# Kernel tuning notes

Hardware: AMD Instinct MI355X
Metric: run time of the kernel (lower is better)

Reference implementation:

```python
import jax, jax.numpy as jnp
import numpy as np

TEMPERATURE = 0.5
EPS = 1e-8  # torch CosineSimilarity eps


def setup_inputs() -> dict:
    key = jax.random.key(0)
    # x holds 2*batch_size concatenated embeddings (two augmented views)
    x = jax.random.normal(key, (4096, 512), dtype=jnp.float32)
    return {"x": x}


def reference(x) -> jnp.ndarray:
    n2 = x.shape[0]          # 2N rows
    n = n2 // 2
    # cosine similarity: normalize rows (clamped norm as in torch), then GEMM
    norms = jnp.maximum(jnp.linalg.norm(x, axis=1, keepdims=True), EPS)
    xn = x / norms
    sim = jnp.einsum('id,jd->ij', xn, xn) / TEMPERATURE  # [2N, 2N]
    # positive logit for row i is sim[i, (i+N) mod 2N]
    idx = jnp.arange(n2)
    pos = sim[idx, (idx + n) % n2]
    # CE with label 0 over logits = [pos, negatives]; since the logit set for
    # row i is exactly {sim[i, j] : j != i}, CE_i = logsumexp_{j!=i} sim[i,j] - pos_i
    sim_masked = jnp.where(jnp.eye(n2, dtype=bool), -jnp.inf, sim)
    lse = jax.nn.logsumexp(sim_masked, axis=1)
    # criterion uses reduction='sum' then divides by bsz -> mean
    return jnp.mean(lse - pos)
```

## Files before the change

### kernel.cpp

```cpp
#include <hip/hip_runtime.h>
#include <hip/hip_bf16.h>
#include <math.h>

typedef __bf16 bf16_t;
typedef __bf16 bf16x8 __attribute__((ext_vector_type(8)));
typedef float f32x4 __attribute__((ext_vector_type(4)));

#define N2 4096
#define NHALF 2048
#define DIM 512
#define TEMP_INV 2.0f

__global__ __launch_bounds__(256) void k_prep(const float* __restrict__ x,
                                              bf16_t* __restrict__ xn,
                                              float* __restrict__ pos,
                                              float* __restrict__ diag,
                                              float* __restrict__ rowsum) {
    const int pair = blockIdx.x * 4 + (threadIdx.x >> 6);
    const int lane = threadIdx.x & 63;
    const int rowi = pair;
    const int rowp = pair + NHALF;

    const float4* xi = reinterpret_cast<const float4*>(x + (size_t)rowi * DIM);
    const float4* xp = reinterpret_cast<const float4*>(x + (size_t)rowp * DIM);
    float4 a0 = xi[lane * 2], a1 = xi[lane * 2 + 1];
    float4 b0 = xp[lane * 2], b1 = xp[lane * 2 + 1];

    float ssi = a0.x*a0.x + a0.y*a0.y + a0.z*a0.z + a0.w*a0.w
              + a1.x*a1.x + a1.y*a1.y + a1.z*a1.z + a1.w*a1.w;
    float ssp = b0.x*b0.x + b0.y*b0.y + b0.z*b0.z + b0.w*b0.w
              + b1.x*b1.x + b1.y*b1.y + b1.z*b1.z + b1.w*b1.w;
    float dot = a0.x*b0.x + a0.y*b0.y + a0.z*b0.z + a0.w*b0.w
              + a1.x*b1.x + a1.y*b1.y + a1.z*b1.z + a1.w*b1.w;
#pragma unroll
    for (int off = 32; off; off >>= 1) {
        ssi += __shfl_xor(ssi, off, 64);
        ssp += __shfl_xor(ssp, off, 64);
        dot += __shfl_xor(dot, off, 64);
    }
    const float ni = fmaxf(sqrtf(ssi), 1e-8f);
    const float np = fmaxf(sqrtf(ssp), 1e-8f);
    const float sci = 1.0f / ni, scp = 1.0f / np;

    float va[8] = {a0.x, a0.y, a0.z, a0.w, a1.x, a1.y, a1.z, a1.w};
    float vb[8] = {b0.x, b0.y, b0.z, b0.w, b1.x, b1.y, b1.z, b1.w};
    bf16x8 oi, op;
    float dii = 0.0f, dpp = 0.0f;
#pragma unroll
    for (int t = 0; t < 8; ++t) {
        oi[t] = (bf16_t)(va[t] * sci);
        op[t] = (bf16_t)(vb[t] * scp);
        float fi = (float)oi[t], fp_ = (float)op[t];
        dii += fi * fi;
        dpp += fp_ * fp_;
    }
    *reinterpret_cast<bf16x8*>(xn + (size_t)rowi * DIM + lane * 8) = oi;
    *reinterpret_cast<bf16x8*>(xn + (size_t)rowp * DIM + lane * 8) = op;
#pragma unroll
    for (int off = 32; off; off >>= 1) {
        dii += __shfl_xor(dii, off, 64);
        dpp += __shfl_xor(dpp, off, 64);
    }
    if (lane == 0) {
        const float pv = TEMP_INV * dot * sci * scp;
        pos[rowi] = pv;
        pos[rowp] = pv;
        diag[rowi] = TEMP_INV * dii;
        diag[rowp] = TEMP_INV * dpp;
    }
    if (threadIdx.x < 8) rowsum[blockIdx.x * 8 + threadIdx.x] = 0.0f;
}

__device__ __forceinline__ void load_lds16(const bf16_t* g, bf16_t* l) {
    __builtin_amdgcn_global_load_lds(
        (const __attribute__((address_space(1))) unsigned int*)g,
        (__attribute__((address_space(3))) unsigned int*)l,
        16, 0, 0);
}

__global__ __launch_bounds__(256) void k_simgemm(const bf16_t* __restrict__ xn,
                                                 float* __restrict__ rowsum) {
    __shared__ bf16_t As[3][128 * 32];
    __shared__ bf16_t Bs[3][128 * 32];
    __shared__ float  rpA[128];
    __shared__ float  rpB[128];

    const int t = blockIdx.x;
    int bn = (int)((sqrtf(8.0f * (float)t + 1.0f) - 1.0f) * 0.5f);
    while ((bn * (bn + 1)) / 2 > t) --bn;
    while (((bn + 1) * (bn + 2)) / 2 <= t) ++bn;
    const int bm = t - (bn * (bn + 1)) / 2;
    const bool diagb = (bm == bn);

    const int tid  = threadIdx.x;
    const int lane = tid & 63;
    const int wid  = tid >> 6;
    const int wr   = wid >> 1;
    const int wc   = wid & 1;
    const int q    = lane >> 4;
    const int l15  = lane & 15;

    if (tid < 128) { rpA[tid] = 0.0f; rpB[tid] = 0.0f; }

    const int slot_g = (tid & 3) ^ ((tid >> 3) & 3);
    const bf16_t* gA = xn + (size_t)(bm * 128 + (tid >> 2)) * DIM + slot_g * 8;
    const bf16_t* gB = xn + (size_t)(bn * 128 + (tid >> 2)) * DIM + slot_g * 8;

    const int rsw = (q ^ ((l15 >> 1) & 3)) * 8;
    const int arow = (wr * 64 + l15) * 32 + rsw;
    const int brow = (wc * 64 + l15) * 32 + rsw;

    f32x4 acc[4][4] = {};

    load_lds16(gA,                         &As[0][tid * 8]);
    load_lds16(gA + (size_t)64 * DIM,      &As[0][2048 + tid * 8]);
    load_lds16(gB,                         &Bs[0][tid * 8]);
    load_lds16(gB + (size_t)64 * DIM,      &Bs[0][2048 + tid * 8]);
    load_lds16(gA + 32,                    &As[1][tid * 8]);
    load_lds16(gA + (size_t)64 * DIM + 32, &As[1][2048 + tid * 8]);
    load_lds16(gB + 32,                    &Bs[1][tid * 8]);
    load_lds16(gB + (size_t)64 * DIM + 32, &Bs[1][2048 + tid * 8]);

#pragma unroll
    for (int kt = 0; kt < 16; ++kt) {
        if (kt < 15) asm volatile("s_waitcnt vmcnt(4)" ::: "memory");
        else         asm volatile("s_waitcnt vmcnt(0)" ::: "memory");
        __builtin_amdgcn_s_barrier();
        __builtin_amdgcn_sched_barrier(0);

        if (kt + 2 < 16) {
            const int nb = (kt + 2) % 3;
            const bf16_t* gA2 = gA + (kt + 2) * 32;
            const bf16_t* gB2 = gB + (kt + 2) * 32;
            load_lds16(gA2,                    &As[nb][tid * 8]);
            load_lds16(gA2 + (size_t)64 * DIM, &As[nb][2048 + tid * 8]);
            load_lds16(gB2,                    &Bs[nb][tid * 8]);
            load_lds16(gB2 + (size_t)64 * DIM, &Bs[nb][2048 + tid * 8]);
        }

        const int cb = kt % 3;
        bf16x8 af[4], bv[4];
#pragma unroll
        for (int mt = 0; mt < 4; ++mt)
            af[mt] = *reinterpret_cast<const bf16x8*>(&As[cb][arow + mt * 512]);
#pragma unroll
        for (int nt = 0; nt < 4; ++nt)
            bv[nt] = *reinterpret_cast<const bf16x8*>(&Bs[cb][brow + nt * 512]);
#pragma unroll
        for (int mt = 0; mt < 4; ++mt)
#pragma unroll
            for (int nt = 0; nt < 4; ++nt)
                acc[mt][nt] = __builtin_amdgcn_mfma_f32_16x16x32_bf16(
                    af[mt], bv[nt], acc[mt][nt], 0, 0, 0);
    }

    float colacc[4] = {0.0f, 0.0f, 0.0f, 0.0f};
#pragma unroll
    for (int mt = 0; mt < 4; ++mt) {
        float rowp[4] = {0.0f, 0.0f, 0.0f, 0.0f};
#pragma unroll
        for (int nt = 0; nt < 4; ++nt)
#pragma unroll
            for (int r = 0; r < 4; ++r) {
                float e = __expf(TEMP_INV * acc[mt][nt][r]);
                rowp[r] += e;
                colacc[nt] += e;
            }
#pragma unroll
        for (int r = 0; r < 4; ++r) {
            float p = rowp[r];
            p += __shfl_xor(p, 1, 64);
            p += __shfl_xor(p, 2, 64);
            p += __shfl_xor(p, 4, 64);
            p += __shfl_xor(p, 8, 64);
            if (l15 == 0) atomicAdd(&rpA[wr * 64 + mt * 16 + q * 4 + r], p);
        }
    }
    if (!diagb) {
#pragma unroll
        for (int nt = 0; nt < 4; ++nt) {
            float c = colacc[nt];
            c += __shfl_xor(c, 16, 64);
            c += __shfl_xor(c, 32, 64);
            if (q == 0) atomicAdd(&rpB[wc * 64 + nt * 16 + l15], c);
        }
    }
    __syncthreads();
    if (tid < 128) {
        atomicAdd(&rowsum[bm * 128 + tid], rpA[tid]);
    } else if (!diagb) {
        atomicAdd(&rowsum[bn * 128 + (tid - 128)], rpB[tid - 128]);
    }
}

__global__ __launch_bounds__(256) void k_finalize(const float* __restrict__ rowsum,
                                                  const float* __restrict__ pos,
                                                  const float* __restrict__ diag,
                                                  float* __restrict__ out) {
    __shared__ float red[256];
    const float4* rs4 = reinterpret_cast<const float4*>(rowsum);
    const float4* ps4 = reinterpret_cast<const float4*>(pos);
    const float4* dg4 = reinterpret_cast<const float4*>(diag);
    float s = 0.0f;
#pragma unroll
    for (int it = 0; it < 4; ++it) {
        const int i = it * 256 + threadIdx.x;
        float4 r = rs4[i];
        float4 p = ps4[i];
        float4 d = dg4[i];
        s += __logf(r.x - __expf(d.x)) - p.x;
        s += __logf(r.y - __expf(d.y)) - p.y;
        s += __logf(r.z - __expf(d.z)) - p.z;
        s += __logf(r.w - __expf(d.w)) - p.w;
    }
    red[threadIdx.x] = s;
    __syncthreads();
    for (int st = 128; st; st >>= 1) {
        if (threadIdx.x < st) red[threadIdx.x] += red[threadIdx.x + st];
        __syncthreads();
    }
    if (threadIdx.x == 0) out[0] = red[0] / (float)N2;
}

extern "C" void kernel_launch(void* const* d_in, const int* in_sizes, int n_in,
                              void* d_out, int out_size, void* d_ws, size_t ws_size,
                              hipStream_t stream) {
    (void)in_sizes; (void)n_in; (void)out_size; (void)ws_size;
    const float* x = (const float*)d_in[0];
    float* out = (float*)d_out;

    char* ws = (char*)d_ws;
    bf16_t* xn     = (bf16_t*)ws;
    float*  rowsum = (float*)(ws + (size_t)N2 * DIM * 2);
    float*  pos    = rowsum + N2;
    float*  diag   = pos + N2;

    k_prep<<<512, 256, 0, stream>>>(x, xn, pos, diag, rowsum);
    k_simgemm<<<528, 256, 0, stream>>>(xn, rowsum);
    k_finalize<<<1, 256, 0, stream>>>(rowsum, pos, diag, out);
}
```

Baseline: 78.77 us.

## Fuse finalize into GEMM via last-block reduction and extract diag/pos from tiles

Removes the separate finalize kernel by having the last GEMM block, found with an atomic counter, do the log-sum reduction. Diagonal terms are now masked to zero inside the GEMM tile instead of being subtracted later from precomputed values. The positive logits are read from the off-diagonal tile at offset 16 blocks instead of being computed in prep, which trims prep work and one kernel launch. The cost is extra branches in the exp epilogue, atomic adds for pos, and a serial tail in the last block.

```diff
diff --git a/kernel.cpp b/kernel.cpp
--- a/kernel.cpp
+++ b/kernel.cpp
@@ -10,12 +10,13 @@
 #define NHALF 2048
 #define DIM 512
 #define TEMP_INV 2.0f
+#define NBLK 528
 
 __global__ __launch_bounds__(256) void k_prep(const float* __restrict__ x,
                                               bf16_t* __restrict__ xn,
                                               float* __restrict__ pos,
-                                              float* __restrict__ diag,
-                                              float* __restrict__ rowsum) {
+                                              float* __restrict__ rowsum,
+                                              int* __restrict__ counter) {
     const int pair = blockIdx.x * 4 + (threadIdx.x >> 6);
     const int lane = threadIdx.x & 63;
     const int rowi = pair;
@@ -30,45 +31,28 @@
               + a1.x*a1.x + a1.y*a1.y + a1.z*a1.z + a1.w*a1.w;
     float ssp = b0.x*b0.x + b0.y*b0.y + b0.z*b0.z + b0.w*b0.w
               + b1.x*b1.x + b1.y*b1.y + b1.z*b1.z + b1.w*b1.w;
-    float dot = a0.x*b0.x + a0.y*b0.y + a0.z*b0.z + a0.w*b0.w
-              + a1.x*b1.x + a1.y*b1.y + a1.z*b1.z + a1.w*b1.w;
 #pragma unroll
     for (int off = 32; off; off >>= 1) {
         ssi += __shfl_xor(ssi, off, 64);
         ssp += __shfl_xor(ssp, off, 64);
-        dot += __shfl_xor(dot, off, 64);
-    }
-    const float ni = fmaxf(sqrtf(ssi), 1e-8f);
-    const float np = fmaxf(sqrtf(ssp), 1e-8f);
-    const float sci = 1.0f / ni, scp = 1.0f / np;
+    }
+    const float sci = 1.0f / fmaxf(sqrtf(ssi), 1e-8f);
+    const float scp = 1.0f / fmaxf(sqrtf(ssp), 1e-8f);
 
     float va[8] = {a0.x, a0.y, a0.z, a0.w, a1.x, a1.y, a1.z, a1.w};
     float vb[8] = {b0.x, b0.y, b0.z, b0.w, b1.x, b1.y, b1.z, b1.w};
     bf16x8 oi, op;
-    float dii = 0.0f, dpp = 0.0f;
 #pragma unroll
     for (int t = 0; t < 8; ++t) {
         oi[t] = (bf16_t)(va[t] * sci);
         op[t] = (bf16_t)(vb[t] * scp);
-        float fi = (float)oi[t], fp_ = (float)op[t];
-        dii += fi * fi;
-        dpp += fp_ * fp_;
     }
     *reinterpret_cast<bf16x8*>(xn + (size_t)rowi * DIM + lane * 8) = oi;
     *reinterpret_cast<bf16x8*>(xn + (size_t)rowp * DIM + lane * 8) = op;
-#pragma unroll
-    for (int off = 32; off; off >>= 1) {
-        dii += __shfl_xor(dii, off, 64);
-        dpp += __shfl_xor(dpp, off, 64);
-    }
-    if (lane == 0) {
-        const float pv = TEMP_INV * dot * sci * scp;
-        pos[rowi] = pv;
-        pos[rowp] = pv;
-        diag[rowi] = TEMP_INV * dii;
-        diag[rowp] = TEMP_INV * dpp;
-    }
-    if (threadIdx.x < 8) rowsum[blockIdx.x * 8 + threadIdx.x] = 0.0f;
+
+    if (threadIdx.x < 8)       rowsum[blockIdx.x * 8 + threadIdx.x] = 0.0f;
+    else if (threadIdx.x < 16) pos[blockIdx.x * 8 + threadIdx.x - 8] = 0.0f;
+    if (blockIdx.x == 0 && threadIdx.x == 16) *counter = 0;
 }
 
 __device__ __forceinline__ void load_lds16(const bf16_t* g, bf16_t* l) {
@@ -79,11 +63,16 @@
 }
 
 __global__ __launch_bounds__(256) void k_simgemm(const bf16_t* __restrict__ xn,
-                                                 float* __restrict__ rowsum) {
+                                                 float* __restrict__ rowsum,
+                                                 float* __restrict__ pos,
+                                                 int* __restrict__ counter,
+                                                 float* __restrict__ out) {
     __shared__ bf16_t As[3][128 * 32];
     __shared__ bf16_t Bs[3][128 * 32];
     __shared__ float  rpA[128];
     __shared__ float  rpB[128];
+    __shared__ float  red[256];
+    __shared__ int    lastBlk;
 
     const int t = blockIdx.x;
     int bn = (int)((sqrtf(8.0f * (float)t + 1.0f) - 1.0f) * 0.5f);
@@ -154,6 +143,8 @@
                     af[mt], bv[nt], acc[mt][nt], 0, 0, 0);
     }
 
+    const bool dmask = diagb && (wr == wc);
+    const bool pmask = (bn == bm + 16) && (wr == wc);
     float colacc[4] = {0.0f, 0.0f, 0.0f, 0.0f};
 #pragma unroll
     for (int mt = 0; mt < 4; ++mt) {
@@ -163,6 +154,16 @@
 #pragma unroll
             for (int r = 0; r < 4; ++r) {
                 float e = __expf(TEMP_INV * acc[mt][nt][r]);
+                if (mt == nt) {
+                    const bool hit = (l15 == q * 4 + r);
+                    if (dmask && hit) e = 0.0f;
+                    if (pmask && hit) {
+                        const float pv = TEMP_INV * acc[mt][nt][r];
+                        const int gr = bm * 128 + wr * 64 + mt * 16 + q * 4 + r;
+                        atomicAdd(&pos[gr], pv);
+                        atomicAdd(&pos[gr + NHALF], pv);
+                    }
+                }
                 rowp[r] += e;
                 colacc[nt] += e;
             }
@@ -191,35 +192,27 @@
     } else if (!diagb) {
         atomicAdd(&rowsum[bn * 128 + (tid - 128)], rpB[tid - 128]);
     }
-}
-
-__global__ __launch_bounds__(256) void k_finalize(const float* __restrict__ rowsum,
-                                                  const float* __restrict__ pos,
-                                                  const float* __restrict__ diag,
-                                                  float* __restrict__ out) {
-    __shared__ float red[256];
-    const float4* rs4 = reinterpret_cast<const float4*>(rowsum);
-    const float4* ps4 = reinterpret_cast<const float4*>(pos);
-    const float4* dg4 = reinterpret_cast<const float4*>(diag);
+
+    __syncthreads();
+    if (tid == 0) lastBlk = (atomicAdd(counter, 1) == NBLK - 1);
+    __syncthreads();
+    if (!lastBlk) return;
+
     float s = 0.0f;
 #pragma unroll
-    for (int it = 0; it < 4; ++it) {
-        const int i = it * 256 + threadIdx.x;
-        float4 r = rs4[i];
-        float4 p = ps4[i];
-        float4 d = dg4[i];
-        s += __logf(r.x - __expf(d.x)) - p.x;
-        s += __logf(r.y - __expf(d.y)) - p.y;
-        s += __logf(r.z - __expf(d.z)) - p.z;
-        s += __logf(r.w - __expf(d.w)) - p.w;
-    }
-    red[threadIdx.x] = s;
+    for (int it = 0; it < 16; ++it) {
+        const int i = it * 256 + tid;
+        float rsv = atomicAdd(&rowsum[i], 0.0f);
+        float pv  = atomicAdd(&pos[i], 0.0f);
+        s += __logf(rsv) - pv;
+    }
+    red[tid] = s;
     __syncthreads();
     for (int st = 128; st; st >>= 1) {
-        if (threadIdx.x < st) red[threadIdx.x] += red[threadIdx.x + st];
+        if (tid < st) red[tid] += red[tid + st];
         __syncthreads();
     }
-    if (threadIdx.x == 0) out[0] = red[0] / (float)N2;
+    if (tid == 0) out[0] = red[0] / (float)N2;
 }
 
 extern "C" void kernel_launch(void* const* d_in, const int* in_sizes, int n_in,
@@ -230,12 +223,11 @@
     float* out = (float*)d_out;
 
     char* ws = (char*)d_ws;
-    bf16_t* xn     = (bf16_t*)ws;
-    float*  rowsum = (float*)(ws + (size_t)N2 * DIM * 2);
-    float*  pos    = rowsum + N2;
-    float*  diag   = pos + N2;
-
-    k_prep<<<512, 256, 0, stream>>>(x, xn, pos, diag, rowsum);
-    k_simgemm<<<528, 256, 0, stream>>>(xn, rowsum);
-    k_finalize<<<1, 256, 0, stream>>>(rowsum, pos, diag, out);
-}
+    bf16_t* xn      = (bf16_t*)ws;
+    float*  rowsum  = (float*)(ws + (size_t)N2 * DIM * 2);
+    float*  pos     = rowsum + N2;
+    int*    counter = (int*)(pos + N2);
+
+    k_prep<<<512, 256, 0, stream>>>(x, xn, pos, rowsum, counter);
+    k_simgemm<<<528, 256, 0, stream>>>(xn, rowsum, pos, counter, out);
+}
```

New measurement: 88.94 us. 1.13x slower.
